# Optimization experiments

Measured on AMD Instinct MI355X. Metric: run time of the kernel, lower is better.

The kernel has to match this reference:

```python
import jax, jax.numpy as jnp
import numpy as np

FILTERS = 64
HIDDEN = 128
T_PRED = 24
DILATIONS = (1, 2, 4, 8, 16, 32)
N_DIL = len(DILATIONS)
FEAT = 15
B = 1024
L_ENC = 168


def setup_inputs() -> dict:
    key = jax.random.key(0)
    ks = jax.random.split(key, 16)
    s = 0.05
    d_in = 1 + FEAT  # prev_output (1) concat current feature
    inp = {
        "decoder_features": jax.random.normal(ks[0], (B, T_PRED, FEAT), jnp.float32),
        "decoder_init_input": jax.random.normal(ks[1], (B, 1), jnp.float32),
        "encoder_states": jax.random.normal(ks[2], (N_DIL, B, L_ENC, FILTERS), jnp.float32),
        # dense_1: d_in -> filters (tanh)
        "W1": jax.random.normal(ks[3], (d_in, FILTERS), jnp.float32) * s,
        "b1": jnp.zeros((FILTERS,), jnp.float32),
        # dense_2: filters -> 2*filters (bias)
        "W2": jax.random.normal(ks[4], (FILTERS, 2 * FILTERS), jnp.float32) * s,
        "b2": jnp.zeros((2 * FILTERS,), jnp.float32),
        # dense_3: filters -> 2*filters (no bias)
        "W3": jax.random.normal(ks[5], (FILTERS, 2 * FILTERS), jnp.float32) * s,
        # dense_4: filters -> 2*filters (bias)
        "W4": jax.random.normal(ks[6], (FILTERS, 2 * FILTERS), jnp.float32) * s,
        "b4": jnp.zeros((2 * FILTERS,), jnp.float32),
        # dense_5: n_dil*filters -> hidden (relu)
        "W5": jax.random.normal(ks[7], (N_DIL * FILTERS, HIDDEN), jnp.float32) * s,
        "b5": jnp.zeros((HIDDEN,), jnp.float32),
        # dense_6: hidden -> 1
        "W6": jax.random.normal(ks[8], (HIDDEN, 1), jnp.float32) * s,
        "b6": jnp.zeros((1,), jnp.float32),
    }
    return inp


def _decode(decoder_features, decoder_init_input, encoder_states,
            W1, b1, W2, b2, W3, W4, b4, W5, b5, W6, b6):
    L = encoder_states.shape[2]
    # 'appended' holds the inputs written back into each dilation's state
    # (the growing-concat part of encoder_states in the original loop).
    appended0 = jnp.zeros((N_DIL, decoder_features.shape[0], T_PRED, FILTERS),
                          dtype=decoder_features.dtype)

    def step(carry, t):
        prev, appended = carry
        cur = jnp.concatenate([prev, decoder_features[:, t, :]], axis=1)  # [B, 1+FEAT]
        inputs = jnp.tanh(cur @ W1 + b1)  # [B, F]
        skips_list = []
        for i, d in enumerate(DILATIONS):
            # grown-state read index is (L + t) - d; if t >= d it lands in the
            # appended region (step t-d), otherwise in the original encoder state.
            idx_app = jnp.clip(t - d, 0, T_PRED - 1)
            idx_orig = jnp.clip(L + t - d, 0, L - 1)
            st_app = jax.lax.dynamic_index_in_dim(appended[i], idx_app, axis=1, keepdims=False)
            st_orig = jax.lax.dynamic_index_in_dim(encoder_states[i], idx_orig, axis=1, keepdims=False)
            state = jnp.where(t >= d, st_app, st_orig)  # [B, F]
            dilated = state @ W2 + b2 + inputs @ W3  # [B, 2F]
            conv_filter, conv_gate = dilated[:, :FILTERS], dilated[:, FILTERS:]
            gated = jnp.tanh(conv_filter) * jax.nn.sigmoid(conv_gate)
            out = gated @ W4 + b4  # [B, 2F]
            skips, residuals = out[:, :FILTERS], out[:, FILTERS:]
            inputs = inputs + residuals
            appended = appended.at[i, :, t, :].set(inputs)
            skips_list.append(skips)
        skip = jax.nn.relu(jnp.concatenate(skips_list, axis=1))  # [B, N_DIL*F]
        h = jax.nn.relu(skip @ W5 + b5)
        y = h @ W6 + b6  # [B, 1]
        return (y, appended), y

    (_, _), ys = jax.lax.scan(step, (decoder_init_input, appended0),
                              jnp.arange(T_PRED))
    return jnp.transpose(ys, (1, 0, 2))  # [B, T, 1]


def reference(decoder_features, decoder_init_input, encoder_states,
              W1, b1, W2, b2, W3, W4, b4, W5, b5, W6, b6):
    return _decode(decoder_features, decoder_init_input, encoder_states,
                   W1, b1, W2, b2, W3, W4, b4, W5, b5, W6, b6)
```

## Files before the change

### kernel.cpp

```cpp
#include <hip/hip_runtime.h>

typedef _Float16 h16;
typedef _Float16 half8 __attribute__((ext_vector_type(8)));
typedef float floatx4 __attribute__((ext_vector_type(4)));

#define B_TOT 1024
#define T_STEPS 24
#define F 64
#define C2 128
#define FEAT 15
#define L_ENC 168
#define HID 128
#define R 16
#define BLK 256
#define FP 72

__device__ __forceinline__ floatx4 mfma16(half8 a, half8 b, floatx4 c) {
  return __builtin_amdgcn_mfma_f32_16x16x32_f16(a, b, c, 0, 0, 0);
}

#define BAR() asm volatile("s_waitcnt lgkmcnt(0)\n\ts_barrier" ::: "memory")

__device__ __forceinline__ float tanh_fast(float x) {
  float cx = fminf(fmaxf(x, -15.f), 15.f);
  float e  = __builtin_amdgcn_exp2f(-2.885390081777927f * cx);
  return (1.f - e) * __builtin_amdgcn_rcpf(1.f + e);
}
__device__ __forceinline__ float gate_fast(float f, float g) {
  float cf = fminf(fmaxf(f, -15.f), 15.f);
  float cg = fminf(fmaxf(g, -30.f), 30.f);
  float ef = __builtin_amdgcn_exp2f(-2.885390081777927f * cf);
  float eg = __builtin_amdgcn_exp2f(-1.4426950408889634f * cg);
  return (1.f - ef) * __builtin_amdgcn_rcpf((1.f + ef) * (1.f + eg));
}

__global__ void prep_w5(const float* __restrict__ gW5, h16* __restrict__ wsW5) {
  int t = blockIdx.x * 256 + threadIdx.x;
  if (t >= 12 * 8 * 64) return;
  int lane = t & 63, nt = (t >> 6) & 7, ktg = t >> 9;
  int n  = nt * 16 + (lane & 15);
  int kb = ktg * 32 + (lane >> 4) * 8;
  half8 v;
  #pragma unroll
  for (int j = 0; j < 8; ++j) v[j] = (h16)gW5[(size_t)(kb + j) * C2 + n];
  *(half8*)&wsW5[(size_t)t * 8] = v;
}

__global__ __launch_bounds__(BLK, 1) void decoder_v7(
    const float* __restrict__ dec_feat,
    const float* __restrict__ dec_init,
    const float* __restrict__ enc,
    const float* __restrict__ gW1, const float* __restrict__ gb1,
    const float* __restrict__ gW2, const float* __restrict__ gb2,
    const float* __restrict__ gW3,
    const float* __restrict__ gW4, const float* __restrict__ gb4,
    const h16*  __restrict__ wsW5, const float* __restrict__ gb5,
    const float* __restrict__ gW6, const float* __restrict__ gb6,
    float* __restrict__ out)
{
  __shared__ alignas(16) h16 ringL[31][R][FP];
  __shared__ alignas(16) h16 xH[R][FP];
  __shared__ alignas(16) h16 gatedH[R][FP];
  __shared__ alignas(16) h16 skipH[R][FP];
  __shared__ alignas(16) h16 curH[R][40];
  __shared__ float ypart[4][R];

  const int tid  = threadIdx.x;
  const int w    = tid >> 6;
  const int lane = tid & 63;
  const int m16  = lane & 15;
  const int q    = lane >> 4;
  const int q8   = q * 8;
  const int b0   = blockIdx.x * R;
  const int col  = w * 16 + m16;
  const int mm0  = tid / FEAT;
  const int f0   = tid - mm0 * FEAT;
  const bool featT = (tid < R * FEAT);

  half8 rW1;
  #pragma unroll
  for (int j = 0; j < 8; ++j) {
    int k = q8 + j;
    rW1[j] = (k < 16) ? (h16)gW1[k * F + col] : (h16)0.0f;
  }
  half8 rW2[2][2], rW3[2][2], rW4[2][2];
  #pragma unroll
  for (int h = 0; h < 2; ++h) {
    int n = (w + 4 * h) * 16 + m16;
    #pragma unroll
    for (int kt = 0; kt < 2; ++kt) {
      half8 v2, v3, v4;
      #pragma unroll
      for (int j = 0; j < 8; ++j) {
        int k = kt * 32 + q8 + j;
        v2[j] = (h16)gW2[k * C2 + n];
        v3[j] = (h16)gW3[k * C2 + n];
        v4[j] = (h16)gW4[k * C2 + n];
      }
      rW2[h][kt] = v2; rW3[h][kt] = v3; rW4[h][kt] = v4;
    }
  }
  half8 w5r[6][4];
  #pragma unroll
  for (int i = 0; i < 6; ++i)
    #pragma unroll
    for (int kt = 0; kt < 2; ++kt)
      #pragma unroll
      for (int nn = 0; nn < 2; ++nn)
        w5r[i][kt * 2 + nn] =
            *(const half8*)&wsW5[(size_t)((((2 * i + kt) * 8) + (w + 4 * nn)) * 64 + lane) * 8];

  const float rb1  = gb1[col];
  const float rb2f = gb2[col], rb2g = gb2[64 + col];
  const float rb4s = gb4[col], rb4r = gb4[64 + col];
  const float rb5a = gb5[col], rb5b = gb5[64 + col];
  const float rw6a = gW6[col], rw6b = gW6[64 + col];
  const float rb6  = gb6[0];

  { int mm = tid >> 4, kk = 16 + (tid & 15); curH[mm][kk] = (h16)0.0f; }
  if (featT) curH[mm0][1 + f0] = (h16)dec_feat[(b0 + mm0) * (T_STEPS * FEAT) + f0];
  if (tid < R) curH[tid][0] = (h16)dec_init[b0 + tid];
  __syncthreads();

  const int rbase[6] = {0, 1, 3, 7, 15, 0};

  auto loadStat = [&](half8* dst, int i, int d, int base, int t) {
    if (t >= d) {
      const h16* p = &ringL[base + (t & (d - 1))][m16][0];
      dst[0] = *(const half8*)(p + q8);
      dst[1] = *(const half8*)(p + 32 + q8);
    } else {
      const float* ep = enc + (((size_t)i * B_TOT + b0 + m16) * L_ENC + (L_ENC + t - d)) * F;
      #pragma unroll
      for (int kt = 0; kt < 2; ++kt) {
        float4 e0 = *(const float4*)(ep + kt * 32 + q8);
        float4 e1 = *(const float4*)(ep + kt * 32 + q8 + 4);
        half8 hv;
        hv[0] = (h16)e0.x; hv[1] = (h16)e0.y; hv[2] = (h16)e0.z; hv[3] = (h16)e0.w;
        hv[4] = (h16)e1.x; hv[5] = (h16)e1.y; hv[6] = (h16)e1.z; hv[7] = (h16)e1.w;
        dst[kt] = hv;
      }
    }
  };

  float xr[4];

  for (int t = 0; t < T_STEPS; ++t) {
    float nf = 0.f;
    const bool doFeat = featT && (t + 1 < T_STEPS);
    if (doFeat) nf = dec_feat[(b0 + mm0) * (T_STEPS * FEAT) + (t + 1) * FEAT + f0];

    half8 aCur = *(const half8*)&curH[m16][q8];
    floatx4 accX = {0.f, 0.f, 0.f, 0.f};
    accX = mfma16(aCur, rW1, accX);
    half8 stat[2];
    loadStat(stat, 0, 1, 0, t);
    #pragma unroll
    for (int j = 0; j < 4; ++j) {
      float v = tanh_fast(accX[j] + rb1);
      xr[j] = v;
      xH[q * 4 + j][col] = (h16)v;
    }
    BAR();

    floatx4 hAccA = {0.f, 0.f, 0.f, 0.f};
    floatx4 hAccB = {0.f, 0.f, 0.f, 0.f};

    #pragma unroll
    for (int i = 0; i < 6; ++i) {
      const int d = 1 << i;
      half8 xA0 = *(const half8*)&xH[m16][q8];
      half8 xA1 = *(const half8*)&xH[m16][32 + q8];
      half8 stN[2];
      if (i < 5) loadStat(stN, i + 1, d << 1, rbase[i + 1], t);

      floatx4 aF = {0.f, 0.f, 0.f, 0.f}, aG = {0.f, 0.f, 0.f, 0.f};
      aF = mfma16(stat[0], rW2[0][0], aF);
      aF = mfma16(stat[1], rW2[0][1], aF);
      aF = mfma16(xA0,     rW3[0][0], aF);
      aF = mfma16(xA1,     rW3[0][1], aF);
      aG = mfma16(stat[0], rW2[1][0], aG);
      aG = mfma16(stat[1], rW2[1][1], aG);
      aG = mfma16(xA0,     rW3[1][0], aG);
      aG = mfma16(xA1,     rW3[1][1], aG);
      #pragma unroll
      for (int j = 0; j < 4; ++j)
        gatedH[q * 4 + j][col] = (h16)gate_fast(aF[j] + rb2f, aG[j] + rb2g);
      BAR();

      half8 gA0 = *(const half8*)&gatedH[m16][q8];
      half8 gA1 = *(const half8*)&gatedH[m16][32 + q8];
      floatx4 oS = {0.f, 0.f, 0.f, 0.f}, oR = {0.f, 0.f, 0.f, 0.f};
      oS = mfma16(gA0, rW4[0][0], oS);
      oS = mfma16(gA1, rW4[0][1], oS);
      oR = mfma16(gA0, rW4[1][0], oR);
      oR = mfma16(gA1, rW4[1][1], oR);
      #pragma unroll
      for (int j = 0; j < 4; ++j) {
        int row = q * 4 + j;
        float s = oS[j] + rb4s;
        skipH[row][col] = (h16)fmaxf(s, 0.0f);
        float xn = xr[j] + oR[j] + rb4r;
        xr[j] = xn;
        h16 hx = (h16)xn;
        xH[row][col] = hx;
        if (i < 5) ringL[rbase[i] + (t & (d - 1))][row][col] = hx;
      }
      BAR();

      half8 sk0 = *(const half8*)&skipH[m16][q8];
      half8 sk1 = *(const half8*)&skipH[m16][32 + q8];
      hAccA = mfma16(sk0, w5r[i][0], hAccA);
      hAccA = mfma16(sk1, w5r[i][2], hAccA);
      hAccB = mfma16(sk0, w5r[i][1], hAccB);
      hAccB = mfma16(sk1, w5r[i][3], hAccB);

      if (i < 5) { stat[0] = stN[0]; stat[1] = stN[1]; }
    }

    {
      floatx4 vv;
      #pragma unroll
      for (int j = 0; j < 4; ++j) {
        float ha = fmaxf(hAccA[j] + rb5a, 0.0f);
        float hb = fmaxf(hAccB[j] + rb5b, 0.0f);
        vv[j] = ha * rw6a + hb * rw6b;
      }
      #pragma unroll
      for (int off = 1; off < 16; off <<= 1) {
        #pragma unroll
        for (int j = 0; j < 4; ++j) vv[j] += __shfl_xor(vv[j], off, 16);
      }
      if (m16 == 0) {
        #pragma unroll
        for (int j = 0; j < 4; ++j) ypart[w][q * 4 + j] = vv[j];
      }
    }
    if (doFeat) curH[mm0][1 + f0] = (h16)nf;
    BAR();
    if (tid < R) {
      float y = ypart[0][tid] + ypart[1][tid] + ypart[2][tid] + ypart[3][tid] + rb6;
      out[(b0 + tid) * T_STEPS + t] = y;
      curH[tid][0] = (h16)y;
    }
    BAR();
  }
}

extern "C" void kernel_launch(void* const* d_in, const int* in_sizes, int n_in,
                              void* d_out, int out_size, void* d_ws, size_t ws_size,
                              hipStream_t stream) {
  const float* dec_feat = (const float*)d_in[0];
  const float* dec_init = (const float*)d_in[1];
  const float* enc      = (const float*)d_in[2];
  const float* W1 = (const float*)d_in[3];
  const float* b1 = (const float*)d_in[4];
  const float* W2 = (const float*)d_in[5];
  const float* b2 = (const float*)d_in[6];
  const float* W3 = (const float*)d_in[7];
  const float* W4 = (const float*)d_in[8];
  const float* b4 = (const float*)d_in[9];
  const float* W5 = (const float*)d_in[10];
  const float* b5 = (const float*)d_in[11];
  const float* W6 = (const float*)d_in[12];
  const float* b6 = (const float*)d_in[13];
  float* out = (float*)d_out;
  h16* wsW5 = (h16*)d_ws;

  prep_w5<<<24, 256, 0, stream>>>(W5, wsW5);
  decoder_v7<<<dim3(B_TOT / R), dim3(BLK), 0, stream>>>(
      dec_feat, dec_init, enc, W1, b1, W2, b2, W3, W4, b4, wsW5, b5, W6, b6, out);
}
```

Baseline: 471.5 us.

## Run each batch tile in a single wavefront with transposed MFMA and no barriers

Replaces the 256-thread, four-wavefront block with one 64-lane wavefront per 16-row batch tile. The wavefront computes all 128 output columns using transposed MFMAs with weights held in registers, so every __syncthreads-style barrier disappears. A new prep kernel packs all weights and biases into fp16 MFMA layouts. The W5 fragments are streamed from global memory for each dilation instead of being kept in registers, and the skip connection now reads the residual from the ring buffer. In exchange, each block gets only one wave (64 blocks × 64 threads), so latency hiding is lower and register pressure is heavy; the tanh and sigmoid clamping is also loosened.

```diff
diff --git a/kernel.cpp b/kernel.cpp
--- a/kernel.cpp
+++ b/kernel.cpp
@@ -1,6 +1,7 @@
 #include <hip/hip_runtime.h>
 
 typedef _Float16 h16;
+typedef _Float16 half4 __attribute__((ext_vector_type(4)));
 typedef _Float16 half8 __attribute__((ext_vector_type(8)));
 typedef float floatx4 __attribute__((ext_vector_type(4)));
 
@@ -10,240 +11,328 @@
 #define C2 128
 #define FEAT 15
 #define L_ENC 168
-#define HID 128
 #define R 16
-#define BLK 256
 #define FP 72
+
+#define OFF_W5 0
+#define OFF_W2 49152
+#define OFF_W3 57344
+#define OFF_W4 65536
+#define OFF_W1 73728
+#define OFF_B1 75776
+#define OFF_B2 75840
+#define OFF_B4 75968
+#define OFF_B5 76096
+#define OFF_W6 76224
 
 __device__ __forceinline__ floatx4 mfma16(half8 a, half8 b, floatx4 c) {
   return __builtin_amdgcn_mfma_f32_16x16x32_f16(a, b, c, 0, 0, 0);
 }
 
-#define BAR() asm volatile("s_waitcnt lgkmcnt(0)\n\ts_barrier" ::: "memory")
+#define PIN(x) asm volatile("" : "+v"(x))
 
 __device__ __forceinline__ float tanh_fast(float x) {
-  float cx = fminf(fmaxf(x, -15.f), 15.f);
+  float cx = fmaxf(x, -30.f);
   float e  = __builtin_amdgcn_exp2f(-2.885390081777927f * cx);
   return (1.f - e) * __builtin_amdgcn_rcpf(1.f + e);
 }
 __device__ __forceinline__ float gate_fast(float f, float g) {
-  float cf = fminf(fmaxf(f, -15.f), 15.f);
-  float cg = fminf(fmaxf(g, -30.f), 30.f);
-  float ef = __builtin_amdgcn_exp2f(-2.885390081777927f * cf);
-  float eg = __builtin_amdgcn_exp2f(-1.4426950408889634f * cg);
+  float ef = __builtin_amdgcn_exp2f(-2.885390081777927f * fmaxf(f, -30.f));
+  float eg = __builtin_amdgcn_exp2f(-1.4426950408889634f * fmaxf(g, -80.f));
   return (1.f - ef) * __builtin_amdgcn_rcpf((1.f + ef) * (1.f + eg));
 }
 
-__global__ void prep_w5(const float* __restrict__ gW5, h16* __restrict__ wsW5) {
+__global__ void prep_pack(const float* __restrict__ W1, const float* __restrict__ b1,
+                          const float* __restrict__ W2, const float* __restrict__ b2,
+                          const float* __restrict__ W3, const float* __restrict__ W4,
+                          const float* __restrict__ b4, const float* __restrict__ W5,
+                          const float* __restrict__ b5, const float* __restrict__ W6,
+                          h16* __restrict__ ws) {
   int t = blockIdx.x * 256 + threadIdx.x;
-  if (t >= 12 * 8 * 64) return;
-  int lane = t & 63, nt = (t >> 6) & 7, ktg = t >> 9;
-  int n  = nt * 16 + (lane & 15);
-  int kb = ktg * 32 + (lane >> 4) * 8;
-  half8 v;
-  #pragma unroll
-  for (int j = 0; j < 8; ++j) v[j] = (h16)gW5[(size_t)(kb + j) * C2 + n];
-  *(half8*)&wsW5[(size_t)t * 8] = v;
-}
-
-__global__ __launch_bounds__(BLK, 1) void decoder_v7(
+  if (t < 6144) {
+    int lane = t & 63, nt = (t >> 6) & 7, ktg = t >> 9;
+    int n = nt * 16 + (lane & 15), kb = ktg * 32 + (lane >> 4) * 8;
+    half8 v;
+    #pragma unroll
+    for (int j = 0; j < 8; ++j) v[j] = (h16)W5[(size_t)(kb + j) * C2 + n];
+    *(half8*)&ws[(size_t)t * 8] = v;
+  } else if (t < 9216) {
+    int u = t - 6144, sel = u >> 10, r = u & 1023;
+    int lane = r & 63, nt = (r >> 6) & 7, kt = r >> 9;
+    const float* W = (sel == 0) ? W2 : (sel == 1) ? W3 : W4;
+    int n = nt * 16 + (lane & 15), kb = kt * 32 + (lane >> 4) * 8;
+    half8 v;
+    #pragma unroll
+    for (int j = 0; j < 8; ++j) v[j] = (h16)W[(size_t)(kb + j) * C2 + n];
+    *(half8*)&ws[OFF_W2 + sel * 8192 + (size_t)r * 8] = v;
+  } else if (t < 9472) {
+    int u = t - 9216, lane = u & 63, nt = u >> 6;
+    int n = nt * 16 + (lane & 15);
+    half8 v;
+    #pragma unroll
+    for (int j = 0; j < 8; ++j) {
+      int k = (lane >> 4) * 8 + j;
+      v[j] = (k < 16) ? (h16)W1[k * F + n] : (h16)0.0f;
+    }
+    *(half8*)&ws[OFF_W1 + (size_t)u * 8] = v;
+  } else if (t < 10048) {
+    int u = t - 9472;
+    h16 v; int off;
+    if (u < 64)       { v = (h16)b1[u];        off = OFF_B1 + u; }
+    else if (u < 192) { v = (h16)b2[u - 64];   off = OFF_B2 + (u - 64); }
+    else if (u < 320) { v = (h16)b4[u - 192];  off = OFF_B4 + (u - 192); }
+    else if (u < 448) { v = (h16)b5[u - 320];  off = OFF_B5 + (u - 320); }
+    else              { v = (h16)W6[u - 448];  off = OFF_W6 + (u - 448); }
+    ws[off] = v;
+  }
+}
+
+__global__ __launch_bounds__(64, 1) void decoder_v11(
     const float* __restrict__ dec_feat,
     const float* __restrict__ dec_init,
     const float* __restrict__ enc,
-    const float* __restrict__ gW1, const float* __restrict__ gb1,
-    const float* __restrict__ gW2, const float* __restrict__ gb2,
-    const float* __restrict__ gW3,
-    const float* __restrict__ gW4, const float* __restrict__ gb4,
-    const h16*  __restrict__ wsW5, const float* __restrict__ gb5,
-    const float* __restrict__ gW6, const float* __restrict__ gb6,
+    const h16*  __restrict__ ws,
+    const float* __restrict__ gb6,
     float* __restrict__ out)
 {
   __shared__ alignas(16) h16 ringL[31][R][FP];
-  __shared__ alignas(16) h16 xH[R][FP];
-  __shared__ alignas(16) h16 gatedH[R][FP];
-  __shared__ alignas(16) h16 skipH[R][FP];
-  __shared__ alignas(16) h16 curH[R][40];
-  __shared__ float ypart[4][R];
-
-  const int tid  = threadIdx.x;
-  const int w    = tid >> 6;
-  const int lane = tid & 63;
+  __shared__ alignas(16) h16 xS[R][FP];
+  __shared__ alignas(16) h16 gatedS[R][FP];
+  __shared__ alignas(16) h16 skipS[R][FP];
+
+  const int lane = threadIdx.x;
   const int m16  = lane & 15;
   const int q    = lane >> 4;
   const int q8   = q * 8;
   const int b0   = blockIdx.x * R;
-  const int col  = w * 16 + m16;
-  const int mm0  = tid / FEAT;
-  const int f0   = tid - mm0 * FEAT;
-  const bool featT = (tid < R * FEAT);
-
-  half8 rW1;
-  #pragma unroll
-  for (int j = 0; j < 8; ++j) {
-    int k = q8 + j;
-    rW1[j] = (k < 16) ? (h16)gW1[k * F + col] : (h16)0.0f;
+  const floatx4 z4 = {0.f, 0.f, 0.f, 0.f};
+
+  half8 rW2[8][2], rW3[8][2], rW4[8][2], rW1[4];
+  #pragma unroll
+  for (int nt = 0; nt < 8; ++nt)
+    #pragma unroll
+    for (int kt = 0; kt < 2; ++kt) {
+      int idx = ((kt * 8 + nt) * 64 + lane) * 8;
+      rW2[nt][kt] = *(const half8*)&ws[OFF_W2 + idx];
+      rW3[nt][kt] = *(const half8*)&ws[OFF_W3 + idx];
+      rW4[nt][kt] = *(const half8*)&ws[OFF_W4 + idx];
+    }
+  #pragma unroll
+  for (int nt = 0; nt < 4; ++nt) rW1[nt] = *(const half8*)&ws[OFF_W1 + (nt * 64 + lane) * 8];
+  half4 b1h[4], b2h[8], b4h[8];
+  #pragma unroll
+  for (int nt = 0; nt < 4; ++nt) b1h[nt] = *(const half4*)&ws[OFF_B1 + nt * 16 + q * 4];
+  #pragma unroll
+  for (int nt = 0; nt < 8; ++nt) {
+    b2h[nt] = *(const half4*)&ws[OFF_B2 + nt * 16 + q * 4];
+    b4h[nt] = *(const half4*)&ws[OFF_B4 + nt * 16 + q * 4];
   }
-  half8 rW2[2][2], rW3[2][2], rW4[2][2];
-  #pragma unroll
-  for (int h = 0; h < 2; ++h) {
-    int n = (w + 4 * h) * 16 + m16;
-    #pragma unroll
-    for (int kt = 0; kt < 2; ++kt) {
-      half8 v2, v3, v4;
-      #pragma unroll
-      for (int j = 0; j < 8; ++j) {
-        int k = kt * 32 + q8 + j;
-        v2[j] = (h16)gW2[k * C2 + n];
-        v3[j] = (h16)gW3[k * C2 + n];
-        v4[j] = (h16)gW4[k * C2 + n];
-      }
-      rW2[h][kt] = v2; rW3[h][kt] = v3; rW4[h][kt] = v4;
-    }
-  }
-  half8 w5r[6][4];
-  #pragma unroll
-  for (int i = 0; i < 6; ++i)
-    #pragma unroll
-    for (int kt = 0; kt < 2; ++kt)
-      #pragma unroll
-      for (int nn = 0; nn < 2; ++nn)
-        w5r[i][kt * 2 + nn] =
-            *(const half8*)&wsW5[(size_t)((((2 * i + kt) * 8) + (w + 4 * nn)) * 64 + lane) * 8];
-
-  const float rb1  = gb1[col];
-  const float rb2f = gb2[col], rb2g = gb2[64 + col];
-  const float rb4s = gb4[col], rb4r = gb4[64 + col];
-  const float rb5a = gb5[col], rb5b = gb5[64 + col];
-  const float rw6a = gW6[col], rw6b = gW6[64 + col];
-  const float rb6  = gb6[0];
-
-  { int mm = tid >> 4, kk = 16 + (tid & 15); curH[mm][kk] = (h16)0.0f; }
-  if (featT) curH[mm0][1 + f0] = (h16)dec_feat[(b0 + mm0) * (T_STEPS * FEAT) + f0];
-  if (tid < R) curH[tid][0] = (h16)dec_init[b0 + tid];
-  __syncthreads();
-
-  const int rbase[6] = {0, 1, 3, 7, 15, 0};
-
-  auto loadStat = [&](half8* dst, int i, int d, int base, int t) {
-    if (t >= d) {
-      const h16* p = &ringL[base + (t & (d - 1))][m16][0];
-      dst[0] = *(const half8*)(p + q8);
-      dst[1] = *(const half8*)(p + 32 + q8);
+  half8 w5f[2][8];
+  #pragma unroll
+  for (int kt = 0; kt < 2; ++kt)
+    #pragma unroll
+    for (int nt = 0; nt < 8; ++nt)
+      w5f[kt][nt] = *(const half8*)&ws[OFF_W5 + ((kt * 8 + nt) * 64 + lane) * 8];
+
+  const float rb6 = gb6[0];
+  float yv = dec_init[b0 + m16];
+
+  const int DD[6]    = {1, 2, 4, 8, 16, 32};
+  const int DBASE[6] = {0, 1, 3, 7, 15, 0};
+
+  float4 e0[4];
+  { const float* ep = enc + (((size_t)0 * B_TOT + b0 + m16) * L_ENC + (L_ENC - 1)) * F + q8;
+    e0[0] = *(const float4*)ep;        e0[1] = *(const float4*)(ep + 4);
+    e0[2] = *(const float4*)(ep + 32); e0[3] = *(const float4*)(ep + 36); }
+
+  #pragma unroll 1
+  for (int t = 0; t < T_STEPS; ++t) {
+    #pragma unroll
+    for (int nt = 0; nt < 8; ++nt)
+      #pragma unroll
+      for (int kt = 0; kt < 2; ++kt) { PIN(rW2[nt][kt]); PIN(rW3[nt][kt]); PIN(rW4[nt][kt]); }
+    #pragma unroll
+    for (int nt = 0; nt < 4; ++nt) PIN(rW1[nt]);
+
+    float fbuf[8];
+    if (q < 2) {
+      const float* fp = dec_feat + (size_t)(b0 + m16) * (T_STEPS * FEAT) + t * FEAT;
+      if (q == 0) {
+        fbuf[0] = 0.f;
+        #pragma unroll
+        for (int j = 1; j < 8; ++j) fbuf[j] = fp[j - 1];
+      } else {
+        #pragma unroll
+        for (int j = 0; j < 8; ++j) fbuf[j] = fp[7 + j];
+      }
+    }
+
+    half8 statc0, statc1;
+    if (t == 0) {
+      #pragma unroll
+      for (int j = 0; j < 4; ++j) { statc0[j] = (h16)e0[0][j]; statc0[4 + j] = (h16)e0[1][j];
+                                    statc1[j] = (h16)e0[2][j]; statc1[4 + j] = (h16)e0[3][j]; }
     } else {
-      const float* ep = enc + (((size_t)i * B_TOT + b0 + m16) * L_ENC + (L_ENC + t - d)) * F;
-      #pragma unroll
-      for (int kt = 0; kt < 2; ++kt) {
-        float4 e0 = *(const float4*)(ep + kt * 32 + q8);
-        float4 e1 = *(const float4*)(ep + kt * 32 + q8 + 4);
-        half8 hv;
-        hv[0] = (h16)e0.x; hv[1] = (h16)e0.y; hv[2] = (h16)e0.z; hv[3] = (h16)e0.w;
-        hv[4] = (h16)e1.x; hv[5] = (h16)e1.y; hv[6] = (h16)e1.z; hv[7] = (h16)e1.w;
-        dst[kt] = hv;
-      }
-    }
-  };
-
-  float xr[4];
-
-  for (int t = 0; t < T_STEPS; ++t) {
-    float nf = 0.f;
-    const bool doFeat = featT && (t + 1 < T_STEPS);
-    if (doFeat) nf = dec_feat[(b0 + mm0) * (T_STEPS * FEAT) + (t + 1) * FEAT + f0];
-
-    half8 aCur = *(const half8*)&curH[m16][q8];
-    floatx4 accX = {0.f, 0.f, 0.f, 0.f};
-    accX = mfma16(aCur, rW1, accX);
-    half8 stat[2];
-    loadStat(stat, 0, 1, 0, t);
-    #pragma unroll
-    for (int j = 0; j < 4; ++j) {
-      float v = tanh_fast(accX[j] + rb1);
-      xr[j] = v;
-      xH[q * 4 + j][col] = (h16)v;
-    }
-    BAR();
-
-    floatx4 hAccA = {0.f, 0.f, 0.f, 0.f};
-    floatx4 hAccB = {0.f, 0.f, 0.f, 0.f};
+      const h16* sr = &ringL[0][m16][0];
+      statc0 = *(const half8*)(sr + q8);
+      statc1 = *(const half8*)(sr + 32 + q8);
+    }
+
+    half8 bCur;
+    if (q == 0) {
+      bCur[0] = (h16)yv;
+      #pragma unroll
+      for (int j = 1; j < 8; ++j) bCur[j] = (h16)fbuf[j];
+    } else if (q == 1) {
+      #pragma unroll
+      for (int j = 0; j < 8; ++j) bCur[j] = (h16)fbuf[j];
+    } else {
+      #pragma unroll
+      for (int j = 0; j < 8; ++j) bCur[j] = (h16)0.0f;
+    }
+    floatx4 xr4[4];
+    {
+      floatx4 aX[4];
+      #pragma unroll
+      for (int nt = 0; nt < 4; ++nt) aX[nt] = mfma16(rW1[nt], bCur, z4);
+      #pragma unroll
+      for (int nt = 0; nt < 4; ++nt) {
+        half4 xv;
+        #pragma unroll
+        for (int j = 0; j < 4; ++j) {
+          float v = tanh_fast(aX[nt][j] + (float)b1h[nt][j]);
+          xr4[nt][j] = v;
+          xv[j] = (h16)v;
+        }
+        *(half4*)&xS[m16][nt * 16 + q * 4] = xv;
+      }
+    }
+
+    floatx4 hacc[8];
+    #pragma unroll
+    for (int nt = 0; nt < 8; ++nt) hacc[nt] = z4;
 
     #pragma unroll
     for (int i = 0; i < 6; ++i) {
-      const int d = 1 << i;
-      half8 xA0 = *(const half8*)&xH[m16][q8];
-      half8 xA1 = *(const half8*)&xH[m16][32 + q8];
-      half8 stN[2];
-      if (i < 5) loadStat(stN, i + 1, d << 1, rbase[i + 1], t);
-
-      floatx4 aF = {0.f, 0.f, 0.f, 0.f}, aG = {0.f, 0.f, 0.f, 0.f};
-      aF = mfma16(stat[0], rW2[0][0], aF);
-      aF = mfma16(stat[1], rW2[0][1], aF);
-      aF = mfma16(xA0,     rW3[0][0], aF);
-      aF = mfma16(xA1,     rW3[0][1], aF);
-      aG = mfma16(stat[0], rW2[1][0], aG);
-      aG = mfma16(stat[1], rW2[1][1], aG);
-      aG = mfma16(xA0,     rW3[1][0], aG);
-      aG = mfma16(xA1,     rW3[1][1], aG);
-      #pragma unroll
-      for (int j = 0; j < 4; ++j)
-        gatedH[q * 4 + j][col] = (h16)gate_fast(aF[j] + rb2f, aG[j] + rb2g);
-      BAR();
-
-      half8 gA0 = *(const half8*)&gatedH[m16][q8];
-      half8 gA1 = *(const half8*)&gatedH[m16][32 + q8];
-      floatx4 oS = {0.f, 0.f, 0.f, 0.f}, oR = {0.f, 0.f, 0.f, 0.f};
-      oS = mfma16(gA0, rW4[0][0], oS);
-      oS = mfma16(gA1, rW4[0][1], oS);
-      oR = mfma16(gA0, rW4[1][0], oR);
-      oR = mfma16(gA1, rW4[1][1], oR);
-      #pragma unroll
-      for (int j = 0; j < 4; ++j) {
-        int row = q * 4 + j;
-        float s = oS[j] + rb4s;
-        skipH[row][col] = (h16)fmaxf(s, 0.0f);
-        float xn = xr[j] + oR[j] + rb4r;
-        xr[j] = xn;
-        h16 hx = (h16)xn;
-        xH[row][col] = hx;
-        if (i < 5) ringL[rbase[i] + (t & (d - 1))][row][col] = hx;
-      }
-      BAR();
-
-      half8 sk0 = *(const half8*)&skipH[m16][q8];
-      half8 sk1 = *(const half8*)&skipH[m16][32 + q8];
-      hAccA = mfma16(sk0, w5r[i][0], hAccA);
-      hAccA = mfma16(sk1, w5r[i][2], hAccA);
-      hAccB = mfma16(sk0, w5r[i][1], hAccB);
-      hAccB = mfma16(sk1, w5r[i][3], hAccB);
-
-      if (i < 5) { stat[0] = stN[0]; stat[1] = stN[1]; }
+      const int d = DD[i];
+      const h16* xrow = (i == 0) ? &xS[m16][0]
+                                 : &ringL[DBASE[i - 1] + (t & (DD[i - 1] - 1))][m16][0];
+      half8 xB0 = *(const half8*)(xrow + q8);
+      half8 xB1 = *(const half8*)(xrow + 32 + q8);
+
+      floatx4 aD[8];
+      #pragma unroll
+      for (int nt = 0; nt < 8; ++nt) aD[nt] = mfma16(rW2[nt][0], statc0, z4);
+      #pragma unroll
+      for (int nt = 0; nt < 8; ++nt) aD[nt] = mfma16(rW2[nt][1], statc1, aD[nt]);
+
+      half8 stN0, stN1; float4 eN[4]; bool nextEnc = false;
+      if (i < 5) {
+        if (t >= DD[i + 1]) {
+          const h16* sr = &ringL[DBASE[i + 1] + (t & (DD[i + 1] - 1))][m16][0];
+          stN0 = *(const half8*)(sr + q8);
+          stN1 = *(const half8*)(sr + 32 + q8);
+        } else {
+          nextEnc = true;
+          const float* ep = enc + (((size_t)(i + 1) * B_TOT + b0 + m16) * L_ENC
+                                   + (L_ENC + t - DD[i + 1])) * F + q8;
+          eN[0] = *(const float4*)ep;        eN[1] = *(const float4*)(ep + 4);
+          eN[2] = *(const float4*)(ep + 32); eN[3] = *(const float4*)(ep + 36);
+        }
+      }
+
+      #pragma unroll
+      for (int nt = 0; nt < 8; ++nt) aD[nt] = mfma16(rW3[nt][0], xB0, aD[nt]);
+      #pragma unroll
+      for (int nt = 0; nt < 8; ++nt) aD[nt] = mfma16(rW3[nt][1], xB1, aD[nt]);
+
+      #pragma unroll
+      for (int nt = 0; nt < 4; ++nt) {
+        half4 gv;
+        #pragma unroll
+        for (int j = 0; j < 4; ++j) {
+          float f = aD[nt][j]     + (float)b2h[nt][j];
+          float g = aD[nt + 4][j] + (float)b2h[nt + 4][j];
+          gv[j] = (h16)gate_fast(f, g);
+        }
+        *(half4*)&gatedS[m16][nt * 16 + q * 4] = gv;
+      }
+      half8 gB0 = *(const half8*)&gatedS[m16][q8];
+      half8 gB1 = *(const half8*)&gatedS[m16][32 + q8];
+
+      floatx4 oD[8];
+      #pragma unroll
+      for (int nt = 0; nt < 8; ++nt) oD[nt] = mfma16(rW4[nt][0], gB0, z4);
+      #pragma unroll
+      for (int nt = 0; nt < 8; ++nt) oD[nt] = mfma16(rW4[nt][1], gB1, oD[nt]);
+
+      #pragma unroll
+      for (int nt = 0; nt < 4; ++nt) {
+        half4 sv;
+        #pragma unroll
+        for (int j = 0; j < 4; ++j)
+          sv[j] = (h16)fmaxf(oD[nt][j] + (float)b4h[nt][j], 0.0f);
+        *(half4*)&skipS[m16][nt * 16 + q * 4] = sv;
+      }
+      if (i < 5) {
+        h16* rrow = &ringL[DBASE[i] + (t & (d - 1))][m16][0];
+        #pragma unroll
+        for (int nt = 0; nt < 4; ++nt) {
+          half4 xv2;
+          #pragma unroll
+          for (int j = 0; j < 4; ++j) {
+            float xn = xr4[nt][j] + oD[nt + 4][j] + (float)b4h[nt + 4][j];
+            xr4[nt][j] = xn;
+            xv2[j] = (h16)xn;
+          }
+          *(half4*)&rrow[nt * 16 + q * 4] = xv2;
+        }
+      }
+      half8 sk0 = *(const half8*)&skipS[m16][q8];
+      half8 sk1 = *(const half8*)&skipS[m16][32 + q8];
+
+      #pragma unroll
+      for (int nt = 0; nt < 8; ++nt) hacc[nt] = mfma16(w5f[0][nt], sk0, hacc[nt]);
+      #pragma unroll
+      for (int nt = 0; nt < 8; ++nt) hacc[nt] = mfma16(w5f[1][nt], sk1, hacc[nt]);
+
+      {
+        const int ln = (i < 5) ? i + 1 : 0;
+        #pragma unroll
+        for (int kt = 0; kt < 2; ++kt)
+          #pragma unroll
+          for (int nt = 0; nt < 8; ++nt)
+            w5f[kt][nt] =
+                *(const half8*)&ws[OFF_W5 + (((2 * ln + kt) * 8 + nt) * 64 + lane) * 8];
+      }
+
+      if (i < 5) {
+        if (!nextEnc) { statc0 = stN0; statc1 = stN1; }
+        else {
+          #pragma unroll
+          for (int j = 0; j < 4; ++j) {
+            statc0[j] = (h16)eN[0][j]; statc0[4 + j] = (h16)eN[1][j];
+            statc1[j] = (h16)eN[2][j]; statc1[4 + j] = (h16)eN[3][j];
+          }
+        }
+      }
     }
 
     {
-      floatx4 vv;
-      #pragma unroll
-      for (int j = 0; j < 4; ++j) {
-        float ha = fmaxf(hAccA[j] + rb5a, 0.0f);
-        float hb = fmaxf(hAccB[j] + rb5b, 0.0f);
-        vv[j] = ha * rw6a + hb * rw6b;
-      }
-      #pragma unroll
-      for (int off = 1; off < 16; off <<= 1) {
-        #pragma unroll
-        for (int j = 0; j < 4; ++j) vv[j] += __shfl_xor(vv[j], off, 16);
-      }
-      if (m16 == 0) {
-        #pragma unroll
-        for (int j = 0; j < 4; ++j) ypart[w][q * 4 + j] = vv[j];
-      }
-    }
-    if (doFeat) curH[mm0][1 + f0] = (h16)nf;
-    BAR();
-    if (tid < R) {
-      float y = ypart[0][tid] + ypart[1][tid] + ypart[2][tid] + ypart[3][tid] + rb6;
-      out[(b0 + tid) * T_STEPS + t] = y;
-      curH[tid][0] = (h16)y;
-    }
-    BAR();
+      float yacc = 0.f;
+      #pragma unroll
+      for (int nt = 0; nt < 8; ++nt) {
+        half4 b5h = *(const half4*)&ws[OFF_B5 + nt * 16 + q * 4];
+        half4 w6h = *(const half4*)&ws[OFF_W6 + nt * 16 + q * 4];
+        #pragma unroll
+        for (int j = 0; j < 4; ++j)
+          yacc += fmaxf(hacc[nt][j] + (float)b5h[j], 0.0f) * (float)w6h[j];
+      }
+      yacc += __shfl_xor(yacc, 16);
+      yacc += __shfl_xor(yacc, 32);
+      yv = yacc + rb6;
+      if (q == 0) out[(size_t)(b0 + m16) * T_STEPS + t] = yv;
+    }
   }
 }
 
@@ -265,9 +354,9 @@
   const float* W6 = (const float*)d_in[12];
   const float* b6 = (const float*)d_in[13];
   float* out = (float*)d_out;
-  h16* wsW5 = (h16*)d_ws;
-
-  prep_w5<<<24, 256, 0, stream>>>(W5, wsW5);
-  decoder_v7<<<dim3(B_TOT / R), dim3(BLK), 0, stream>>>(
-      dec_feat, dec_init, enc, W1, b1, W2, b2, W3, W4, b4, wsW5, b5, W6, b6, out);
-}
+  h16* wsp = (h16*)d_ws;
+
+  prep_pack<<<40, 256, 0, stream>>>(W1, b1, W2, b2, W3, W4, b4, W5, b5, W6, wsp);
+  decoder_v11<<<dim3(B_TOT / R), dim3(64), 0, stream>>>(
+      dec_feat, dec_init, enc, wsp, b6, out);
+}
```

Result: slower. 1.156 ms (+145.3%).
